# Kernel optimization log

Measured on AMD Instinct MI355X. Metric: run time of the kernel, lower is better.

Reference implementation:

```python
import jax, jax.numpy as jnp
import numpy as np

VOCAB = 41      # len(MOL_DICT) + 1
EMB = 512       # EMBEDDING_SIZE
HID = 1024
B, T = 128, 256


def setup_inputs() -> dict:
    key = jax.random.key(0)
    ks = jax.random.split(key, 8)
    x = jax.random.randint(ks[0], (B, T), 0, VOCAB)
    # realistic prefix padding mask: True for valid tokens, False for padding
    lengths = jax.random.randint(ks[1], (B,), T // 4, T + 1)
    padding_mask = jnp.arange(T)[None, :] < lengths[:, None]
    s = 0.05
    emb_table = jax.random.normal(ks[2], (VOCAB, EMB), jnp.float32) * s
    gru_kernel = jax.random.normal(ks[3], (EMB, 3 * HID), jnp.float32) * s
    gru_rec_kernel = jax.random.normal(ks[4], (HID, 3 * HID), jnp.float32) * s
    gru_bias = jax.random.normal(ks[5], (2, 3 * HID), jnp.float32) * s
    dense_w = jax.random.normal(ks[6], (HID, VOCAB), jnp.float32) * s
    dense_b = jnp.zeros((VOCAB,), jnp.float32)
    return {"x": x, "padding_mask": padding_mask, "emb_table": emb_table,
            "gru_kernel": gru_kernel, "gru_rec_kernel": gru_rec_kernel,
            "gru_bias": gru_bias, "dense_w": dense_w, "dense_b": dense_b}


def _gru_scan(x_proj_t, mask_t, rec_kernel, rec_bias):
    # x_proj_t: [T, B, 3H] precomputed input projections; mask_t: [T, B] bool
    def step(h, inp):
        xp, m = inp                      # xp: [B, 3H], m: [B]
        rec = h @ rec_kernel + rec_bias  # [B, 3H]  (reset_after=True)
        xz, xr, xh = jnp.split(xp, 3, axis=-1)
        rz, rr, rh = jnp.split(rec, 3, axis=-1)
        z = jax.nn.sigmoid(xz + rz)
        r = jax.nn.sigmoid(xr + rr)
        hh = jnp.tanh(xh + r * rh)
        h_new = z * h + (1.0 - z) * hh
        # masked steps carry previous state/output forward (keras semantics)
        h = jnp.where(m[:, None], h_new, h)
        return h, h

    h0 = jnp.zeros((x_proj_t.shape[1], HID), x_proj_t.dtype)
    _, outs = jax.lax.scan(step, h0, (x_proj_t, mask_t))
    return outs  # [T, B, H]


def reference(x, padding_mask, emb_table, gru_kernel, gru_rec_kernel,
              gru_bias, dense_w, dense_b):
    xe = emb_table[x]                              # [B, T, E]
    x_proj = xe @ gru_kernel + gru_bias[0]         # [B, T, 3H]
    outs = _gru_scan(jnp.transpose(x_proj, (1, 0, 2)),
                     jnp.transpose(padding_mask, (1, 0)),
                     gru_rec_kernel, gru_bias[1])  # [T, B, H]
    h = jnp.transpose(outs, (1, 0, 2))             # [B, T, H]
    logits = h @ dense_w + dense_b                 # [B, T, VOCAB]
    return logits
```

## Files before the change

kernel.cpp:

```cpp
#include <hip/hip_runtime.h>
#include <stdint.h>
#include <stddef.h>

#define VOCAB 41
#define EMB   512
#define HID   1024
#define H3    3072
#define BB    128
#define TT    256
#define BT    (BB*TT)
#define NSLOT 3
#define SLOT_U32 8192

typedef unsigned short u16;
typedef uint32_t u32;
typedef _Float16 half_t;
typedef half_t f16x8 __attribute__((ext_vector_type(8)));
typedef float f32x4 __attribute__((ext_vector_type(4)));
typedef u32 u32x4 __attribute__((ext_vector_type(4)));

__device__ __forceinline__ float bf2f(u16 u) {
  return __uint_as_float(((uint32_t)u) << 16);
}
__device__ __forceinline__ u16 f2bf(float f) {
  uint32_t x = __float_as_uint(f);
  return (u16)((x + 0x7FFFu + ((x >> 16) & 1u)) >> 16);
}
__device__ __forceinline__ u16 f2h_bits(float f) {
  half_t h = (half_t)f;
  return __builtin_bit_cast(u16, h);
}
__device__ __forceinline__ float sigmoidf_(float x) {
  return 1.0f / (1.0f + __expf(-x));
}
__device__ __forceinline__ float tanh_fast(float x) {
  return 1.0f - 2.0f / (__expf(2.0f * x) + 1.0f);
}


__global__ void detect_kernel(const u16* __restrict__ raw, int* __restrict__ flag) {
  __shared__ int s[256];
  int tid = threadIdx.x, cnt = 0;
  for (int i = tid; i < 4096; i += 256) {
    int e = (raw[i] >> 7) & 0xFF;
    if (e >= 132) cnt++;
  }
  s[tid] = cnt; __syncthreads();
  if (tid == 0) {
    int tot = 0;
    for (int i = 0; i < 256; i++) tot += s[i];
    *flag = (tot > 4) ? 1 : 0;
  }
}

__global__ void conv_kernel(const void* __restrict__ src, float* __restrict__ dst,
                            int n, const int* __restrict__ flag) {
  int i = blockIdx.x * 256 + threadIdx.x;
  if (i >= n) return;
  if (*flag) dst[i] = ((const float*)src)[i];
  else       dst[i] = bf2f(((const u16*)src)[i]);
}

__global__ void tokm_kernel(const int* __restrict__ x,
                            const unsigned char* __restrict__ m,
                            int* __restrict__ tokm) {
  int i = blockIdx.x * 256 + threadIdx.x;
  unsigned char b0 = m[0], b1 = m[1];
  bool t;
  if (b0 == 1) {
    if (b1 != 0) t = (m[i] != 0);
    else         t = (((const int*)m)[i] != 0);
  } else if (b0 == 0x80) {
    t = (((const u16*)m)[i] != 0);
  } else {
    t = (((const float*)m)[i] != 0.0f);
  }
  tokm[i] = x[i] | (t ? 0 : 0x80000000);
}

__global__ __launch_bounds__(256) void proj_kernel(
    const void* __restrict__ emb, const void* __restrict__ gk,
    const float* __restrict__ gbf, float* __restrict__ P,
    const int* __restrict__ flag) {
  int v = blockIdx.x / (H3 / 256);
  int j = (blockIdx.x % (H3 / 256)) * 256 + threadIdx.x;
  float acc = gbf[j];
  if (*flag) {
    const float* e = (const float*)emb + v * EMB;
    const float* g = (const float*)gk;
    for (int k = 0; k < EMB; ++k) acc = fmaf(e[k], g[k * H3 + j], acc);
  } else {
    const u16* e = (const u16*)emb + v * EMB;
    const u16* g = (const u16*)gk;
    for (int k = 0; k < EMB; ++k) acc = fmaf(bf2f(e[k]), bf2f(g[k * H3 + j]), acc);
  }
  P[v * H3 + j] = acc;
}

__global__ void p2_kernel(const float* __restrict__ P, const float* __restrict__ gbf,
                          float* __restrict__ P2) {
  int gc = blockIdx.x;
  int v = threadIdx.x;
  if (v >= VOCAB) return;
  float val = P[v * H3 + gc];
  if (gc < 2048) val += gbf[H3 + gc];
  P2[gc * VOCAB + v] = val;
}

__global__ void pack_wimg_kernel(const void* __restrict__ src, u16* __restrict__ img,
                                 const int* __restrict__ flag) {
  int idx = blockIdx.x * 256 + threadIdx.x;
  int j = idx & 7;
  int t1 = idx >> 3;
  int lane = t1 & 63;
  int t2 = t1 >> 6;
  int c = t2 % 6;
  int t3 = t2 / 6;
  int ks = t3 & 31;
  int ds = t3 >> 5;
  int g = c >> 1, dh = c & 1;
  int k = ks * 32 + (lane >> 4) * 8 + j;
  int col = g * 1024 + ds * 32 + dh * 16 + (lane & 15);
  float val;
  if (*flag) val = ((const float*)src)[(size_t)k * H3 + col];
  else       val = bf2f(((const u16*)src)[(size_t)k * H3 + col]);
  img[idx] = f2h_bits(val);
}

__global__ void pack_dimg_kernel(const void* __restrict__ src, u16* __restrict__ img,
                                 const int* __restrict__ flag) {
  int idx = blockIdx.x * 256 + threadIdx.x;
  int j = idx & 7;
  int t1 = idx >> 3;
  int lane = t1 & 63;
  int t2 = t1 >> 6;
  int ct = t2 % 3;
  int ks = t2 / 3;
  int k = ks * 32 + (lane >> 4) * 8 + j;
  int v = ct * 16 + (lane & 15);
  float val = 0.0f;
  if (v < VOCAB) {
    if (*flag) val = ((const float*)src)[(size_t)k * VOCAB + v];
    else       val = bf2f(((const u16*)src)[(size_t)k * VOCAB + v]);
  }
  img[idx] = f2h_bits(val);
}

__global__ __launch_bounds__(256, 1) void gru_persist(
    const uint4* __restrict__ Wimg, const int* __restrict__ tokm,
    const float* __restrict__ P2, const float* __restrict__ gbf,
    u32* __restrict__ exch, u16* __restrict__ Hout,
    int* __restrict__ rolectl) {
  int tid = threadIdx.x;
  int w = tid >> 6, lane = tid & 63;

  __shared__ float red[4][64][25];
  __shared__ __align__(16) u16 tr[512];
  __shared__ float Pl[3][32][41];
  __shared__ int tokL[16 * 259];
  __shared__ int roleS;

  if (tid == 0) {
    u32 xcd;
    asm volatile("s_getreg_b32 %0, hwreg(HW_REG_XCC_ID)" : "=s"(xcd));
    xcd &= 7;
    int r = __hip_atomic_fetch_add(rolectl + xcd, 1, __ATOMIC_RELAXED,
                                   __HIP_MEMORY_SCOPE_AGENT);
    int role;
    if (r < 32) role = (int)xcd * 32 + r;
    else {
      int o = __hip_atomic_fetch_add(rolectl + 8, 1, __ATOMIC_RELAXED,
                                     __HIP_MEMORY_SCOPE_AGENT);
      role = -2 - o;
    }
    __hip_atomic_fetch_add(rolectl + 9, 1, __ATOMIC_RELAXED,
                           __HIP_MEMORY_SCOPE_AGENT);
    while (__hip_atomic_load(rolectl + 9, __ATOMIC_RELAXED,
                             __HIP_MEMORY_SCOPE_AGENT) < 256)
      __builtin_amdgcn_s_sleep(8);
    if (role < 0) {
      int o = -2 - role, seen = 0;
      for (int g = 0; g < 8; ++g) {
        int c = __hip_atomic_load(rolectl + g, __ATOMIC_RELAXED,
                                  __HIP_MEMORY_SCOPE_AGENT);
        int cc = c > 32 ? 32 : c;
        int nf = 32 - cc;
        if (o < seen + nf) { role = g * 32 + cc + (o - seen); break; }
        seen += nf;
      }
    }
    int cg = __hip_atomic_load(rolectl + (role >> 5), __ATOMIC_RELAXED,
                               __HIP_MEMORY_SCOPE_AGENT);
    int dirty = (cg < 32) ? 1 : 0;
    roleS = role | (dirty << 16);
  }
  __syncthreads();
  int role = roleS & 0xFFFF;
  int dirty = roleS >> 16;
  int gt = role >> 5, ds = role & 31;

  f16x8 breg[6][8];
  {
    const uint4* wsrc = Wimg + (size_t)ds * (32 * 6) * 64 + lane;
    #pragma unroll
    for (int k8 = 0; k8 < 8; ++k8)
      #pragma unroll
      for (int c = 0; c < 6; ++c)
        breg[c][k8] = __builtin_bit_cast(f16x8, wsrc[((w * 8 + k8) * 6 + c) * 64]);
  }

  for (int i = tid; i < 3 * 32 * VOCAB; i += 256) {
    int v = i % VOCAB;
    int t1 = i / VOCAB;
    int di = t1 & 31, g = t1 >> 5;
    Pl[g][di][v] = P2[(size_t)(g * 1024 + ds * 32 + di) * VOCAB + v];
  }
  for (int i = tid; i < 16 * 256; i += 256) {
    int rr = i >> 8, cc = i & 255;
    tokL[rr * 259 + cc] = tokm[gt * 4096 + i];
  }

  int row = tid >> 4, dimb = tid & 15;
  int lane_src = (row >> 2) * 16 + dimb;
  int rg = row & 3;
  float b1h0 = gbf[H3 + 2048 + ds * 32 + dimb];
  float b1h1 = gbf[H3 + 2048 + ds * 32 + dimb + 16];
  float hc0 = 0.f, hc1 = 0.f;
  __syncthreads();

  int coh = dirty;
  int slot_c = 0, slot_p = 1;
  u32x4 d[8];
  for (int t = 0; t < TT; ++t) {
    const u32* slotb = exch + (size_t)(gt * 3 + slot_c) * SLOT_U32;
    const u32* abase = slotb + (size_t)(w * 8) * 256 + lane * 4;
    const u32* sp = slotb + (size_t)(w * 8 + (lane >> 3)) * 256 +
                    (lane & 7) * 32 + 31;
    u32 texp = ((u32)(t & 1) << 14) | ((u32)(t & 2) << 29);
    int tries = 0;
    while (true) {
      int m = coh & (tries & 1);
      u32 v;
      if (!m)
        asm volatile("global_load_dword %0, %1, off sc0\n\ts_waitcnt vmcnt(0)"
                     : "=v"(v) : "v"(sp) : "memory");
      else
        asm volatile("global_load_dword %0, %1, off sc1\n\ts_waitcnt vmcnt(0)"
                     : "=v"(v) : "v"(sp) : "memory");
      __builtin_amdgcn_sched_barrier(0);
      if (__ballot((v & 0x40004000u) != texp) == 0ULL) {
        if (!m) {
          #pragma unroll
          for (int i = 0; i < 8; ++i)
            asm volatile("global_load_dwordx4 %0, %1, off sc0"
                         : "=v"(d[i]) : "v"(abase + (size_t)i * 256) : "memory");
        } else {
          #pragma unroll
          for (int i = 0; i < 8; ++i)
            asm volatile("global_load_dwordx4 %0, %1, off sc1"
                         : "=v"(d[i]) : "v"(abase + (size_t)i * 256) : "memory");
        }
        asm volatile("s_waitcnt vmcnt(0)" ::: "memory");
        __builtin_amdgcn_sched_barrier(0);
        u32 bad = 0;
        #pragma unroll
        for (int i = 0; i < 8; ++i) {
          u32x4 q = d[i];
          bad |= (q.x ^ texp) | (q.y ^ texp) | (q.z ^ texp) | (q.w ^ texp);
        }
        bad &= 0x40004000u;
        if (__ballot(bad != 0) == 0ULL) break;
      }
      __builtin_amdgcn_s_sleep(1);
      if (++tries > 512) coh = 1;
      if (tries > (1 << 17)) break;
    }

    f32x4 acc[6];
    #pragma unroll
    for (int c = 0; c < 6; ++c) acc[c] = (f32x4){0.f, 0.f, 0.f, 0.f};
    #pragma unroll
    for (int k8 = 0; k8 < 8; ++k8) {
      u32x4 q = d[k8] & 0xBFFFBFFFu;
      f16x8 a = __builtin_bit_cast(f16x8, q);
      #pragma unroll
      for (int c = 0; c < 6; ++c)
        acc[c] = __builtin_amdgcn_mfma_f32_16x16x32_f16(a, breg[c][k8], acc[c], 0, 0, 0);
    }

    {
      float* q = red[w][lane];
      #pragma unroll
      for (int c = 0; c < 6; ++c)
        #pragma unroll
        for (int r = 0; r < 4; ++r) q[c * 4 + r] = acc[c][r];
    }
    __syncthreads();

    {
      int tm = tokL[row * 259 + t];
      int tok = tm & 0xFFFF;
      #pragma unroll
      for (int dh = 0; dh < 2; ++dh) {
        float a0 = 0.f, a1 = 0.f, a2 = 0.f;
        #pragma unroll
        for (int ww = 0; ww < 4; ++ww) {
          const float* q = red[ww][lane_src];
          a0 += q[(0 * 2 + dh) * 4 + rg];
          a1 += q[(1 * 2 + dh) * 4 + rg];
          a2 += q[(2 * 2 + dh) * 4 + rg];
        }
        int dglob = dimb + dh * 16;
        float z  = sigmoidf_(Pl[0][dglob][tok] + a0);
        float r_ = sigmoidf_(Pl[1][dglob][tok] + a1);
        float b1h = dh ? b1h1 : b1h0;
        float hh = tanh_fast(Pl[2][dglob][tok] + r_ * (a2 + b1h));
        float h = dh ? hc1 : hc0;
        if (tm >= 0) h = z * h + (1.0f - z) * hh;
        if (dh) hc1 = h; else hc0 = h;
        tr[(dglob >> 3) * 128 + row * 8 + (dglob & 7)] = f2h_bits(h);
      }
    }
    __syncthreads();

    if (w == 0) {
      u32x4 tr4 = ((const u32x4*)tr)[lane];
      u32 tmask = ((u32)((t + 1) & 1) << 14) | ((u32)((t + 1) & 2) << 29);
      u32x4 o = tr4 | tmask;
      u32* eb = exch + (size_t)(gt * 3 + slot_p) * SLOT_U32 + ds * 256 + lane * 4;
      if (!dirty)
        asm volatile("global_store_dwordx4 %0, %1, off"
                     :: "v"(eb), "v"(o) : "memory");
      else
        asm volatile("global_store_dwordx4 %0, %1, off sc1"
                     :: "v"(eb), "v"(o) : "memory");
      {
        int quad = lane >> 4, mm = lane & 15;
        int b = gt * 16 + mm;
        size_t idx = ((size_t)(b * 16 + (t >> 4)) * 32 + ds) * 64 +
                     quad * 16 + (t & 15);
        ((u32x4*)Hout)[idx] = tr4;
      }
    }
    slot_c = slot_p;
    slot_p = (slot_p == 2) ? 0 : slot_p + 1;
  }
}

__global__ __launch_bounds__(256) void dense_mfma(
    const u16* __restrict__ HoutImg, const uint4* __restrict__ dimg,
    const float* __restrict__ dbf, void* __restrict__ out,
    const int* __restrict__ flag) {
  __shared__ uint4 Bl[48 * 64];
  int tid = threadIdx.x;
  int w = tid >> 6, lane = tid & 63;
  int quad = lane >> 4, vi = lane & 15;
  int gt0 = blockIdx.x * 8 + w * 2;

  f32x4 acc[2][3];
  #pragma unroll
  for (int i = 0; i < 2; ++i)
    #pragma unroll
    for (int c = 0; c < 3; ++c) acc[i][c] = (f32x4){0.f, 0.f, 0.f, 0.f};

  for (int half = 0; half < 2; ++half) {
    for (int i = tid; i < 48 * 64; i += 256) Bl[i] = dimg[half * 48 * 64 + i];
    __syncthreads();
    #pragma unroll
    for (int ks16 = 0; ks16 < 16; ++ks16) {
      int ks = half * 16 + ks16;
      f16x8 a0 = __builtin_bit_cast(
          f16x8, ((const uint4*)HoutImg)[((size_t)gt0 * 32 + ks) * 64 + lane]);
      f16x8 a1 = __builtin_bit_cast(
          f16x8, ((const uint4*)HoutImg)[(((size_t)gt0 + 1) * 32 + ks) * 64 + lane]);
      #pragma unroll
      for (int c = 0; c < 3; ++c) {
        f16x8 bf = __builtin_bit_cast(f16x8, Bl[(ks16 * 3 + c) * 64 + lane]);
        acc[0][c] = __builtin_amdgcn_mfma_f32_16x16x32_f16(a0, bf, acc[0][c], 0, 0, 0);
        acc[1][c] = __builtin_amdgcn_mfma_f32_16x16x32_f16(a1, bf, acc[1][c], 0, 0, 0);
      }
    }
    __syncthreads();
  }

  int isf = *flag;
  #pragma unroll
  for (int i = 0; i < 2; ++i) {
    #pragma unroll
    for (int c = 0; c < 3; ++c) {
      int v = c * 16 + vi;
      if (v >= VOCAB) continue;
      float bias = dbf[v];
      #pragma unroll
      for (int rg = 0; rg < 4; ++rg) {
        size_t bt = (size_t)(gt0 + i) * 16 + quad * 4 + rg;
        float val = acc[i][c][rg] + bias;
        if (isf) ((float*)out)[bt * VOCAB + v] = val;
        else     ((u16*)out)[bt * VOCAB + v] = f2bf(val);
      }
    }
  }
}


extern "C" void kernel_launch(void* const* d_in, const int* in_sizes, int n_in,
                              void* d_out, int out_size, void* d_ws, size_t ws_size,
                              hipStream_t stream) {
  const int* x            = (const int*)d_in[0];
  const unsigned char* mk = (const unsigned char*)d_in[1];

  char* ws = (char*)d_ws;
  int*   flag    = (int*)(ws + 0);
  float* dbf     = (float*)(ws + 4 * 1024);
  float* gbf     = (float*)(ws + 8 * 1024);
  int*   rolectl = (int*)(ws + 32 * 1024);
  int*   tokm    = (int*)(ws + 64 * 1024);
  u16*   dimg    = (u16*)(ws + 192 * 1024);
  float* P       = (float*)(ws + 288 * 1024);
  float* P2      = (float*)(ws + 800 * 1024);
  u32*   exch    = (u32*)(ws + 1312 * 1024);
  u16*   Wimg    = (u16*)(ws + 3456 * 1024);
  u16*   Hout    = (u16*)(ws + 10 * 1024 * 1024);

  detect_kernel<<<1, 256, 0, stream>>>((const u16*)d_in[4], flag);
  conv_kernel<<<(2 * H3 + 255) / 256, 256, 0, stream>>>(d_in[5], gbf, 2 * H3, flag);
  conv_kernel<<<1, 256, 0, stream>>>(d_in[7], dbf, VOCAB, flag);
  tokm_kernel<<<BT / 256, 256, 0, stream>>>(x, mk, tokm);
  proj_kernel<<<VOCAB * (H3 / 256), 256, 0, stream>>>(d_in[2], d_in[3], gbf, P, flag);
  p2_kernel<<<H3, 64, 0, stream>>>(P, gbf, P2);
  pack_wimg_kernel<<<(32 * 32 * 6 * 64 * 8) / 256, 256, 0, stream>>>(d_in[4], Wimg, flag);
  pack_dimg_kernel<<<(32 * 3 * 64 * 8) / 256, 256, 0, stream>>>(d_in[6], dimg, flag);
  hipMemsetAsync(exch, 0, (size_t)8 * NSLOT * SLOT_U32 * 4, stream);
  hipMemsetAsync(rolectl, 0, 64, stream);

  gru_persist<<<256, 256, 0, stream>>>((const uint4*)Wimg, tokm, P2, gbf,
                                       exch, Hout, rolectl);
  dense_mfma<<<256, 256, 0, stream>>>(Hout, (const uint4*)dimg, dbf, d_out, flag);
}
```

Measured before the change: 1.111 ms.

## Poll per-slice step counters and batch Hout writes every sixteen steps

Each block now publishes a separate monotonic step counter after its exchange store. Waiters poll that small counter array instead of sampling tag bits in the exchange data. Hidden states are buffered in LDS for sixteen timesteps, then written to Hout by all threads in one coalesced burst, taking the global writes off the per-step critical path. The tag validation of the data loads is kept, so a counter seen before the data is visible is still caught. The cost is extra LDS and an extra store per step.

```diff
diff --git a/kernel.cpp b/kernel.cpp
--- a/kernel.cpp
+++ b/kernel.cpp
@@ -150,12 +150,12 @@
     const uint4* __restrict__ Wimg, const int* __restrict__ tokm,
     const float* __restrict__ P2, const float* __restrict__ gbf,
     u32* __restrict__ exch, u16* __restrict__ Hout,
-    int* __restrict__ rolectl) {
+    int* __restrict__ rolectl, u32* __restrict__ db) {
   int tid = threadIdx.x;
   int w = tid >> 6, lane = tid & 63;
 
   __shared__ float red[4][64][25];
-  __shared__ __align__(16) u16 tr[512];
+  __shared__ __align__(16) u16 trH[16 * 512];
   __shared__ float Pl[3][32][41];
   __shared__ int tokL[16 * 259];
   __shared__ int roleS;
@@ -230,25 +230,25 @@
 
   int coh = dirty;
   int slot_c = 0, slot_p = 1;
+  const u32* dbq = db + (size_t)(gt * 4 + w) * 32 + (lane & 7);
   u32x4 d[8];
   for (int t = 0; t < TT; ++t) {
     const u32* slotb = exch + (size_t)(gt * 3 + slot_c) * SLOT_U32;
     const u32* abase = slotb + (size_t)(w * 8) * 256 + lane * 4;
-    const u32* sp = slotb + (size_t)(w * 8 + (lane >> 3)) * 256 +
-                    (lane & 7) * 32 + 31;
     u32 texp = ((u32)(t & 1) << 14) | ((u32)(t & 2) << 29);
+    u32 tth = (u32)t;
     int tries = 0;
     while (true) {
       int m = coh & (tries & 1);
       u32 v;
       if (!m)
         asm volatile("global_load_dword %0, %1, off sc0\n\ts_waitcnt vmcnt(0)"
-                     : "=v"(v) : "v"(sp) : "memory");
+                     : "=v"(v) : "v"(dbq) : "memory");
       else
         asm volatile("global_load_dword %0, %1, off sc1\n\ts_waitcnt vmcnt(0)"
-                     : "=v"(v) : "v"(sp) : "memory");
+                     : "=v"(v) : "v"(dbq) : "memory");
       __builtin_amdgcn_sched_barrier(0);
-      if (__ballot((v & 0x40004000u) != texp) == 0ULL) {
+      if (__ballot(v < tth) == 0ULL) {
         if (!m) {
           #pragma unroll
           for (int i = 0; i < 8; ++i)
@@ -300,6 +300,7 @@
     {
       int tm = tokL[row * 259 + t];
       int tok = tm & 0xFFFF;
+      u16* trc = trH + (t & 15) * 512;
       #pragma unroll
       for (int dh = 0; dh < 2; ++dh) {
         float a0 = 0.f, a1 = 0.f, a2 = 0.f;
@@ -318,13 +319,13 @@
         float h = dh ? hc1 : hc0;
         if (tm >= 0) h = z * h + (1.0f - z) * hh;
         if (dh) hc1 = h; else hc0 = h;
-        tr[(dglob >> 3) * 128 + row * 8 + (dglob & 7)] = f2h_bits(h);
+        trc[(dglob >> 3) * 128 + row * 8 + (dglob & 7)] = f2h_bits(h);
       }
     }
     __syncthreads();
 
     if (w == 0) {
-      u32x4 tr4 = ((const u32x4*)tr)[lane];
+      u32x4 tr4 = ((const u32x4*)trH)[(t & 15) * 64 + lane];
       u32 tmask = ((u32)((t + 1) & 1) << 14) | ((u32)((t + 1) & 2) << 29);
       u32x4 o = tr4 | tmask;
       u32* eb = exch + (size_t)(gt * 3 + slot_p) * SLOT_U32 + ds * 256 + lane * 4;
@@ -334,12 +335,30 @@
       else
         asm volatile("global_store_dwordx4 %0, %1, off sc1"
                      :: "v"(eb), "v"(o) : "memory");
-      {
-        int quad = lane >> 4, mm = lane & 15;
-        int b = gt * 16 + mm;
-        size_t idx = ((size_t)(b * 16 + (t >> 4)) * 32 + ds) * 64 +
-                     quad * 16 + (t & 15);
-        ((u32x4*)Hout)[idx] = tr4;
+      if (lane == 0) {
+        u32* dbp = db + (size_t)(gt * 4 + (ds >> 3)) * 32 + (ds & 7);
+        u32 val = (u32)(t + 1);
+        if (!dirty)
+          asm volatile("global_store_dword %0, %1, off"
+                       :: "v"(dbp), "v"(val) : "memory");
+        else
+          asm volatile("global_store_dword %0, %1, off sc1"
+                       :: "v"(dbp), "v"(val) : "memory");
+      }
+    }
+
+    if ((t & 15) == 15) {
+      int c = tid >> 4, s = tid & 15;
+      int T4 = t >> 4;
+      int b = gt * 16 + c;
+      const u32x4* src = (const u32x4*)trH;
+      u32x4* dstv = (u32x4*)Hout;
+      size_t dbase = ((size_t)(b * 16 + T4) * 32 + ds) * 64;
+      #pragma unroll
+      for (int k = 0; k < 4; ++k) {
+        int e = s * 4 + k;
+        int quad = e >> 4, t15 = e & 15;
+        dstv[dbase + e] = src[t15 * 64 + quad * 16 + c];
       }
     }
     slot_c = slot_p;
@@ -414,6 +433,7 @@
   float* dbf     = (float*)(ws + 4 * 1024);
   float* gbf     = (float*)(ws + 8 * 1024);
   int*   rolectl = (int*)(ws + 32 * 1024);
+  u32*   db      = (u32*)(ws + 48 * 1024);
   int*   tokm    = (int*)(ws + 64 * 1024);
   u16*   dimg    = (u16*)(ws + 192 * 1024);
   float* P       = (float*)(ws + 288 * 1024);
@@ -432,8 +452,9 @@
   pack_dimg_kernel<<<(32 * 3 * 64 * 8) / 256, 256, 0, stream>>>(d_in[6], dimg, flag);
   hipMemsetAsync(exch, 0, (size_t)8 * NSLOT * SLOT_U32 * 4, stream);
   hipMemsetAsync(rolectl, 0, 64, stream);
+  hipMemsetAsync(db, 0, 4 * 1024, stream);
 
   gru_persist<<<256, 256, 0, stream>>>((const uint4*)Wimg, tokm, P2, gbf,
-                                       exch, Hout, rolectl);
+                                       exch, Hout, rolectl, db);
   dense_mfma<<<256, 256, 0, stream>>>(Hout, (const uint4*)dimg, dbf, d_out, flag);
 }
```

After: 1.003 ms. 1.11x faster.
